# Kernel optimization log

Hardware: AMD Instinct MI355X
Metric: run time of the kernel (lower is better)

Reference implementation:

```python
import jax, jax.numpy as jnp
import numpy as np

N, E, D_IN, D_H, D_OUT, W = 100000, 1600000, 128, 128, 128, 3
HTC_W, TEMP = 0.01, 1.0  # curvature c = 1.0


def _project(x):
    n = jnp.maximum(jnp.linalg.norm(x, axis=-1, keepdims=True), 1e-12)
    return x * jnp.minimum((1.0 - 1e-5) / n, 1.0)


def _artanh(x):
    x = jnp.clip(x, -1.0 + 1e-6, 1.0 - 1e-6)
    return 0.5 * (jnp.log1p(x) - jnp.log1p(-x))


def _expmap0(v):
    n = jnp.maximum(jnp.linalg.norm(v, axis=-1, keepdims=True), 1e-12)
    return _project(jnp.tanh(n) * v / n)


def _logmap0(y):
    y = _project(y)
    n = jnp.maximum(jnp.linalg.norm(y, axis=-1, keepdims=True), 1e-12)
    return _artanh(n) * y / n


def setup_inputs() -> dict:
    key = jax.random.key(0)
    ks = jax.random.split(key, 24)
    x = jax.random.normal(ks[0], (N, D_IN), dtype=jnp.float32)
    edge_index = jax.random.randint(ks[1], (2, E), 0, N)
    t = jax.random.uniform(ks[2], (E,), dtype=jnp.float32)
    prev_hyp = _project(jax.random.normal(ks[3], (N, D_OUT), dtype=jnp.float32) * 0.05)
    lengths = jax.random.randint(ks[4], (N,), 0, W + 1)
    valid_mask = jnp.arange(W)[None, :] < lengths[:, None]  # front-filled deque
    hist_hyp = _project(jax.random.normal(ks[5], (N, W, D_OUT), dtype=jnp.float32) * 0.05)
    hist_hyp = hist_hyp * valid_mask[..., None].astype(jnp.float32)  # padded slots are zero

    def lin(k, dout, din):
        return jax.random.normal(k, (dout, din), dtype=jnp.float32) / np.sqrt(din)

    params = dict(
        w_time=jax.random.normal(ks[6], (D_IN,), dtype=jnp.float32),
        b_time=jnp.zeros((D_IN,), jnp.float32),
        W0_l=lin(ks[7], D_H, D_IN), b0_l=jnp.zeros((D_H,), jnp.float32), W0_r=lin(ks[8], D_H, D_IN),
        W1_l=lin(ks[9], D_OUT, D_H), b1_l=jnp.zeros((D_OUT,), jnp.float32), W1_r=lin(ks[10], D_OUT, D_H),
        W_ih=lin(ks[11], 3 * D_OUT, D_OUT), W_hh=lin(ks[12], 3 * D_OUT, D_OUT),
        b_ih=jnp.zeros((3 * D_OUT,), jnp.float32), b_hh=jnp.zeros((3 * D_OUT,), jnp.float32),
        Wq=lin(ks[13], D_OUT, D_OUT), Wk=lin(ks[14], D_OUT, D_OUT), Wv=lin(ks[15], D_OUT, D_OUT),
    )
    return dict(x=x, edge_index=edge_index, t=t, prev_hyp=prev_hyp,
                hist_hyp=hist_hyp, valid_mask=valid_mask, **params)


def reference(x, edge_index, t, prev_hyp, hist_hyp, valid_mask,
              w_time, b_time, W0_l, b0_l, W0_r, W1_l, b1_l, W1_r,
              W_ih, W_hh, b_ih, b_hh, Wq, Wk, Wv):
    n = x.shape[0]
    src, dst = edge_index[0], edge_index[1]
    ones_e = jnp.ones_like(t)
    # per-node mean event time over incident edges (src and dst both count)
    nt = jax.ops.segment_sum(t, src, n) + jax.ops.segment_sum(t, dst, n)
    cnt = jax.ops.segment_sum(ones_e, src, n) + jax.ops.segment_sum(ones_e, dst, n)
    node_time = nt / jnp.maximum(cnt, 1.0)
    x = x + jnp.cos(node_time[:, None] * w_time[None, :] + b_time[None, :])
    # SAGEConv (mean aggr over incoming edges): out = W_l @ mean_j x_j + b + W_r @ x_i
    deg = jnp.maximum(jax.ops.segment_sum(ones_e, dst, n), 1.0)[:, None]
    agg0 = jax.ops.segment_sum(x[src], dst, n) / deg
    h = jax.nn.relu(agg0 @ W0_l.T + b0_l + x @ W0_r.T)
    agg1 = jax.ops.segment_sum(h[src], dst, n) / deg
    h_now = agg1 @ W1_l.T + b1_l + h @ W1_r.T  # tangent-space current embedding

    prev_tan = _logmap0(prev_hyp)
    # ragged history attention (padded + masked)
    hist_tan = _logmap0(hist_hyp)                       # [N, W, D]
    q = h_now @ Wq.T                                    # [N, D]
    k = hist_tan @ Wk.T                                 # [N, W, D]
    v = hist_tan @ Wv.T
    score = jnp.einsum('nwd,nd->nw', k, q) / (np.sqrt(D_OUT) * max(TEMP, 1e-6))
    has_hist = valid_mask.any(axis=-1, keepdims=True)
    score = jnp.where(valid_mask, score, -jnp.inf)
    score = jnp.where(has_hist, score, 0.0)
    alpha = jax.nn.softmax(score, axis=-1)
    alpha = jnp.where(has_hist, alpha, 0.0)
    ctx = jnp.einsum('nw,nwd->nd', alpha, v)

    # GRUCell(input=h_now, hidden=prev_tan + ctx)
    hidden = prev_tan + ctx
    gi = h_now @ W_ih.T + b_ih
    gh = hidden @ W_hh.T + b_hh
    i_r, i_z, i_n = jnp.split(gi, 3, axis=-1)
    h_r, h_z, h_n = jnp.split(gh, 3, axis=-1)
    r = jax.nn.sigmoid(i_r + h_r)
    z = jax.nn.sigmoid(i_z + h_z)
    nn_ = jnp.tanh(i_n + r * h_n)
    h_tan = (1.0 - z) * nn_ + z * hidden
    h_hyp = _expmap0(h_tan)

    # hyperbolic temporal consistency aux loss (c = 1)
    x_sq = jnp.sum(h_hyp * h_hyp, axis=-1)
    y_sq = jnp.sum(prev_hyp * prev_hyp, axis=-1)
    diff_sq = jnp.sum((h_hyp - prev_hyp) ** 2, axis=-1)
    denom = jnp.maximum((1.0 - x_sq) * (1.0 - y_sq), 1e-8)
    zarg = jnp.maximum(1.0 + 2.0 * diff_sq / denom, 1.0 + 1e-6)
    dist = jnp.arccosh(zarg)
    valid_prev = (jnp.sum(jnp.abs(prev_hyp), axis=-1) > 0).astype(dist.dtype)
    aux = HTC_W * jnp.sum(dist * valid_prev) / jnp.maximum(jnp.sum(valid_prev), 1.0)
    aux = jnp.where(jnp.any(valid_prev > 0), aux, 0.0)
    return h_hyp, aux
```

## Files before the change

### kernel.cpp

```cpp
#include <hip/hip_runtime.h>
#include <math.h>


typedef _Float16 f16x8 __attribute__((ext_vector_type(8)));
typedef _Float16 f16x4 __attribute__((ext_vector_type(4)));
typedef _Float16 f16x2 __attribute__((ext_vector_type(2)));
typedef float f32x4 __attribute__((ext_vector_type(4)));

__device__ __forceinline__ float wsum(float v) {
#pragma unroll
  for (int off = 1; off < 64; off <<= 1) v += __shfl_xor(v, off, 64);
  return v;
}

__device__ __forceinline__ void fsplit(float x, _Float16& h, _Float16& l) {
  h = (_Float16)x;
  l = (_Float16)(x - (float)h);
}

__device__ __forceinline__ float logmap_scale(float nrm2) {
  float n0 = fmaxf(sqrtf(nrm2), 1e-12f);
  float sp = fminf((1.0f - 1e-5f) / n0, 1.0f);
  float np = fmaxf(n0 * sp, 1e-12f);
  float a  = fminf(np, 1.0f - 1e-6f);
  float at = 0.5f * (log1pf(a) - log1pf(-a));
  return sp * at / np;
}

__global__ void k_edge(const int* __restrict__ ei, const float* __restrict__ t,
                       unsigned long long* __restrict__ packed, int E) {
  int e = blockIdx.x * 256 + threadIdx.x;
  if (e >= E) return;
  int s = ei[e], d = ei[E + e];
  unsigned long long tf =
      (unsigned long long)__float2uint_rn(t[e] * 16777216.0f);
  unsigned long long encs = tf | (1ULL << 40);
  atomicAdd(&packed[s], encs);
  atomicAdd(&packed[d], encs | (1ULL << 52));
}

__global__ void k_scan1(const unsigned long long* __restrict__ packed,
                        int* __restrict__ rowptr, int* __restrict__ bsum, int N) {
  __shared__ int s[256];
  int t = threadIdx.x;
  int base = blockIdx.x * 1024 + t * 4;
  int v[4]; int loc = 0;
#pragma unroll
  for (int j = 0; j < 4; ++j) {
    int i = base + j;
    v[j] = (i < N) ? (int)(packed[i] >> 52) : 0;
    loc += v[j];
  }
  s[t] = loc; __syncthreads();
  for (int off = 1; off < 256; off <<= 1) {
    int x = (t >= off) ? s[t - off] : 0; __syncthreads();
    s[t] += x; __syncthreads();
  }
  int run = s[t] - loc;
#pragma unroll
  for (int j = 0; j < 4; ++j) { int i = base + j; if (i < N) rowptr[i] = run; run += v[j]; }
  if (t == 255) bsum[blockIdx.x] = s[255];
}

__global__ void k_scan2(const int* __restrict__ bsum, int* __restrict__ boff, int nb) {
  __shared__ int s[128];
  int t = threadIdx.x;
  int v = (t < nb) ? bsum[t] : 0;
  s[t] = v; __syncthreads();
  for (int off = 1; off < 128; off <<= 1) {
    int x = (t >= off) ? s[t - off] : 0; __syncthreads();
    s[t] += x; __syncthreads();
  }
  boff[t] = s[t] - v;
}

__global__ void k_scan3(int* __restrict__ rowptr, const int* __restrict__ boff, int N, int E) {
  int i = blockIdx.x * 256 + threadIdx.x;
  if (i < N) rowptr[i] += boff[i >> 10];
  if (i == 0) rowptr[N] = E;
}

__global__ void k_scatter(const int* __restrict__ ei, const int* __restrict__ rowptr,
                          int* __restrict__ cursor, int* __restrict__ eidx, int E) {
  int e = blockIdx.x * 256 + threadIdx.x;
  if (e >= E) return;
  int s = ei[e], d = ei[E + e];
  int p = rowptr[d] + atomicAdd(&cursor[d], 1);
  eidx[p] = s;
}

__global__ void k_time(const float* __restrict__ x,
                       const unsigned long long* __restrict__ packed,
                       const float* __restrict__ wt,
                       const float* __restrict__ bt, float* __restrict__ outF,
                       _Float16* __restrict__ outH, _Float16* __restrict__ outL, int N) {
  int id = blockIdx.x * 256 + threadIdx.x;
  if (id >= N * 32) return;
  int n = id >> 5, q = id & 31;
  unsigned long long p = packed[n];
  float tsum = (float)(p & 0xFFFFFFFFFFULL) * 5.9604644775390625e-8f;
  int c = (int)((p >> 40) & 0xFFF);
  float tm = tsum / fmaxf((float)c, 1.0f);
  float4 xv = ((const float4*)x)[id];
  float4 wv = ((const float4*)wt)[q];
  float4 bv = ((const float4*)bt)[q];
  float o[4];
  o[0] = xv.x + cosf(tm * wv.x + bv.x);
  o[1] = xv.y + cosf(tm * wv.y + bv.y);
  o[2] = xv.z + cosf(tm * wv.z + bv.z);
  o[3] = xv.w + cosf(tm * wv.w + bv.w);
  ((float4*)outF)[id] = make_float4(o[0], o[1], o[2], o[3]);
  f16x4 vh, vl;
#pragma unroll
  for (int j = 0; j < 4; ++j) { _Float16 h, l; fsplit(o[j], h, l); vh[j] = h; vl[j] = l; }
  *(f16x4*)&outH[(size_t)id * 4] = vh;
  *(f16x4*)&outL[(size_t)id * 4] = vl;
}

__global__ void k_agg(const float* __restrict__ X, const int* __restrict__ rowptr,
                      const int* __restrict__ eidx, _Float16* __restrict__ outH,
                      _Float16* __restrict__ outL, int N) {
  int wid = threadIdx.x >> 6, lane = threadIdx.x & 63;
  int n = blockIdx.x * 4 + wid;
  if (n >= N) return;
  int s0 = rowptr[n], s1 = rowptr[n + 1];
  float ax = 0.f, ay = 0.f;
  for (int e = s0; e < s1; ++e) {
    int s = eidx[e];
    float2 v = ((const float2*)X)[(size_t)s * 64 + lane];
    ax += v.x; ay += v.y;
  }
  float sc = 1.0f / fmaxf((float)(s1 - s0), 1.0f);
  _Float16 hx, lx, hy, ly;
  fsplit(ax * sc, hx, lx); fsplit(ay * sc, hy, ly);
  f16x2 vh = {hx, hy}, vl = {lx, ly};
  *(f16x2*)&outH[(size_t)n * 128 + lane * 2] = vh;
  *(f16x2*)&outL[(size_t)n * 128 + lane * 2] = vl;
}

__global__ void k_prep(const float* __restrict__ W0l, const float* __restrict__ W0r,
                       const float* __restrict__ W1l, const float* __restrict__ W1r,
                       const float* __restrict__ Wv,  const float* __restrict__ Wih,
                       const float* __restrict__ Whh, const float* __restrict__ bih,
                       const float* __restrict__ bhh,
                       _Float16* __restrict__ W0H, _Float16* __restrict__ W0L,
                       _Float16* __restrict__ W1H, _Float16* __restrict__ W1L,
                       _Float16* __restrict__ WvH, _Float16* __restrict__ WvL,
                       _Float16* __restrict__ WzH, _Float16* __restrict__ WzL,
                       float* __restrict__ bz) {
  int id = blockIdx.x * 256 + threadIdx.x;
  if (id < 32768) {
    int c = id >> 8, k = id & 255;
    float v0 = (k < 128) ? W0l[c * 128 + k] : W0r[c * 128 + (k - 128)];
    float v1 = (k < 128) ? W1l[c * 128 + k] : W1r[c * 128 + (k - 128)];
    fsplit(v0, W0H[id], W0L[id]);
    fsplit(v1, W1H[id], W1L[id]);
  }
  if (id < 16384) {
    fsplit(Wv[id], WvH[id], WvL[id]);
  }
  if (id < 131072) {
    int c = id >> 8, k = id & 255;
    float v;
    if (c < 256)      v = (k < 128) ? Wih[c * 128 + k] : Whh[c * 128 + (k - 128)];
    else if (c < 384) v = (k < 128) ? Wih[c * 128 + k] : 0.f;
    else              v = (k < 128) ? 0.f : Whh[(c - 128) * 128 + (k - 128)];
    fsplit(v, WzH[id], WzL[id]);
  }
  if (id < 512) {
    float v;
    if (id < 256)      v = bih[id] + bhh[id];
    else if (id < 384) v = bih[id];
    else               v = bhh[id - 128];
    bz[id] = v;
  }
}

__global__ void k_ct(const float* __restrict__ Wk, const float* __restrict__ Wq,
                     _Float16* __restrict__ CtH, _Float16* __restrict__ CtL) {
  int id = blockIdx.x * 256 + threadIdx.x;
  if (id >= 16384) return;
  int c = id >> 7, k = id & 127;
  float s = 0.f;
  for (int j = 0; j < 128; ++j) s += Wk[j * 128 + c] * Wq[j * 128 + k];
  fsplit(s, CtH[id], CtL[id]);
}

__global__ __launch_bounds__(256)
void k_mm(const _Float16* __restrict__ A1H, const _Float16* __restrict__ A1L,
          const _Float16* __restrict__ A2H, const _Float16* __restrict__ A2L,
          const _Float16* __restrict__ WH,  const _Float16* __restrict__ WL,
          const float* __restrict__ bias,   const float* __restrict__ addb,
          float* __restrict__ outF, _Float16* __restrict__ outH,
          _Float16* __restrict__ outL,
          int Nrows, int Ktot, int Ctot, int relu) {
  __shared__ _Float16 sA[2][128][64];
  __shared__ _Float16 sW[2][128][64];
  const int tid = threadIdx.x;
  const int lane = tid & 63;
  const int wv = tid >> 6;
  const int wr = wv >> 1, wc = wv & 1;
  const int laneR = lane & 15, laneG = lane >> 4;
  const int n0 = blockIdx.x * 128;
  const int c0 = blockIdx.y * 128;

  f32x4 acc[4][4];
#pragma unroll
  for (int mi = 0; mi < 4; ++mi)
#pragma unroll
    for (int ni = 0; ni < 4; ++ni)
#pragma unroll
      for (int j = 0; j < 4; ++j) acc[mi][ni][j] = 0.f;

  const int nslab = Ktot >> 6;
  for (int s = 0; s < nslab; ++s) {
    int kglob = s << 6;
    const _Float16* aH = (kglob < 128) ? A1H : A2H;
    const _Float16* aL = (kglob < 128) ? A1L : A2L;
    int kc = kglob & 127;
    __syncthreads();
#pragma unroll
    for (int it = 0; it < 4; ++it) {
      int idx = tid + (it << 8);
      int r = idx >> 3, chunk = idx & 7;
      int cs = (chunk ^ (r & 7)) << 3;
      int kq = chunk << 3;
      int n = n0 + r;
      f16x8 vh, vl;
      if (n < Nrows) {
        vh = *(const f16x8*)&aH[(size_t)n * 128 + kc + kq];
        vl = *(const f16x8*)&aL[(size_t)n * 128 + kc + kq];
      } else {
#pragma unroll
        for (int j = 0; j < 8; ++j) { vh[j] = (_Float16)0; vl[j] = (_Float16)0; }
      }
      *(f16x8*)&sA[0][r][cs] = vh;
      *(f16x8*)&sA[1][r][cs] = vl;
      int c = c0 + r;
      f16x8 wh = *(const f16x8*)&WH[(size_t)c * Ktot + kglob + kq];
      f16x8 wl = *(const f16x8*)&WL[(size_t)c * Ktot + kglob + kq];
      *(f16x8*)&sW[0][r][cs] = wh;
      *(f16x8*)&sW[1][r][cs] = wl;
    }
    __syncthreads();
#pragma unroll
    for (int kk = 0; kk < 2; ++kk) {
      f16x8 ah[4], al[4], bh[4], bl[4];
      int kch = (kk << 2) + laneG;
#pragma unroll
      for (int m = 0; m < 4; ++m) {
        int row = wr * 64 + m * 16 + laneR;
        int ko = (kch ^ (row & 7)) << 3;
        ah[m] = *(const f16x8*)&sA[0][row][ko];
        al[m] = *(const f16x8*)&sA[1][row][ko];
      }
#pragma unroll
      for (int n = 0; n < 4; ++n) {
        int row = wc * 64 + n * 16 + laneR;
        int ko = (kch ^ (row & 7)) << 3;
        bh[n] = *(const f16x8*)&sW[0][row][ko];
        bl[n] = *(const f16x8*)&sW[1][row][ko];
      }
#pragma unroll
      for (int m = 0; m < 4; ++m)
#pragma unroll
        for (int n = 0; n < 4; ++n) {
          acc[m][n] = __builtin_amdgcn_mfma_f32_16x16x32_f16(ah[m], bh[n], acc[m][n], 0, 0, 0);
          acc[m][n] = __builtin_amdgcn_mfma_f32_16x16x32_f16(al[m], bh[n], acc[m][n], 0, 0, 0);
          acc[m][n] = __builtin_amdgcn_mfma_f32_16x16x32_f16(ah[m], bl[n], acc[m][n], 0, 0, 0);
        }
    }
  }
#pragma unroll
  for (int m = 0; m < 4; ++m) {
#pragma unroll
    for (int n = 0; n < 4; ++n) {
      int rbase = n0 + wr * 64 + m * 16 + laneG * 4;
      int c = c0 + wc * 64 + n * 16 + laneR;
      float bval = bias ? bias[c] : 0.f;
#pragma unroll
      for (int j = 0; j < 4; ++j) {
        int r = rbase + j;
        if (r >= Nrows) continue;
        float v = acc[m][n][j] + bval;
        if (addb) v += addb[(size_t)r * Ctot + c];
        if (relu) v = fmaxf(v, 0.f);
        if (outF) outF[(size_t)r * Ctot + c] = v;
        if (outH) {
          _Float16 h, l; fsplit(v, h, l);
          outH[(size_t)r * Ctot + c] = h;
          outL[(size_t)r * Ctot + c] = l;
        }
      }
    }
  }
}

__global__ __launch_bounds__(256, 2)
void k_gru(const _Float16* __restrict__ P0H, const _Float16* __restrict__ P0L,
           const _Float16* __restrict__ P2H, const _Float16* __restrict__ P2L,
           const _Float16* __restrict__ WzH, const _Float16* __restrict__ WzL,
           const float* __restrict__ bz, const float* __restrict__ prev,
           float* __restrict__ out, float* __restrict__ pd,
           float* __restrict__ pv, int N) {
  __shared__ _Float16 sA[2][64][64];
  __shared__ float rn1[64][2];
  __shared__ float rn3[64][2][3];
  __shared__ float distrow[64], validrow[64];
  const int tid = threadIdx.x;
  const int lane = tid & 63;
  const int wv = tid >> 6;
  const int wr = wv >> 1, wc = wv & 1;
  const int laneR = lane & 15, laneG = lane >> 4;
  const int n0 = blockIdx.x * 64;

  f32x4 acc[4][2][4];
#pragma unroll
  for (int q = 0; q < 4; ++q)
#pragma unroll
    for (int m = 0; m < 2; ++m)
#pragma unroll
      for (int n = 0; n < 4; ++n)
#pragma unroll
        for (int j = 0; j < 4; ++j) acc[q][m][n][j] = 0.f;

#define COMPUTE_Q(Q)                                                        \
  {                                                                         \
    _Pragma("unroll")                                                       \
    for (int kk = 0; kk < 2; ++kk) {                                        \
      int kch = (kk << 2) + laneG;                                          \
      f16x8 ah[2], al[2], bh[4], bl[4];                                     \
      _Pragma("unroll")                                                     \
      for (int n = 0; n < 4; ++n) {                                         \
        size_t wrow = (size_t)((Q) * 128 + wc * 64 + n * 16 + laneR);       \
        size_t o = wrow * 256 + kglob + (kch << 3);                         \
        bh[n] = *(const f16x8*)&WzH[o];                                     \
        bl[n] = *(const f16x8*)&WzL[o];                                     \
      }                                                                     \
      _Pragma("unroll")                                                     \
      for (int m = 0; m < 2; ++m) {                                         \
        int row = wr * 32 + m * 16 + laneR;                                 \
        int ko = (kch ^ (row & 7)) << 3;                                    \
        ah[m] = *(const f16x8*)&sA[0][row][ko];                             \
        al[m] = *(const f16x8*)&sA[1][row][ko];                             \
      }                                                                     \
      _Pragma("unroll")                                                     \
      for (int m = 0; m < 2; ++m)                                           \
        _Pragma("unroll")                                                   \
        for (int n = 0; n < 4; ++n) {                                       \
          acc[Q][m][n] = __builtin_amdgcn_mfma_f32_16x16x32_f16(ah[m], bh[n], acc[Q][m][n], 0, 0, 0); \
          acc[Q][m][n] = __builtin_amdgcn_mfma_f32_16x16x32_f16(al[m], bh[n], acc[Q][m][n], 0, 0, 0); \
          acc[Q][m][n] = __builtin_amdgcn_mfma_f32_16x16x32_f16(ah[m], bl[n], acc[Q][m][n], 0, 0, 0); \
        }                                                                   \
    }                                                                       \
  }

#pragma unroll
  for (int s = 0; s < 4; ++s) {
    int kglob = s << 6;
    const _Float16* aH = (s < 2) ? P0H : P2H;
    const _Float16* aL = (s < 2) ? P0L : P2L;
    int kc = kglob & 127;
    __syncthreads();
#pragma unroll
    for (int it = 0; it < 2; ++it) {
      int idx = tid + (it << 8);
      int r = idx >> 3, chunk = idx & 7;
      int cs = (chunk ^ (r & 7)) << 3;
      int kq = chunk << 3;
      int n = n0 + r;
      f16x8 vh, vl;
      if (n < N) {
        vh = *(const f16x8*)&aH[(size_t)n * 128 + kc + kq];
        vl = *(const f16x8*)&aL[(size_t)n * 128 + kc + kq];
      } else {
#pragma unroll
        for (int j = 0; j < 8; ++j) { vh[j] = (_Float16)0; vl[j] = (_Float16)0; }
      }
      *(f16x8*)&sA[0][r][cs] = vh;
      *(f16x8*)&sA[1][r][cs] = vl;
    }
    __syncthreads();
    COMPUTE_Q(0);
    COMPUTE_Q(1);
    if (s < 2) {
      COMPUTE_Q(2);
    } else {
      COMPUTE_Q(3);
    }
  }
#undef COMPUTE_Q

  float bz0[4], bz1[4], bz2[4], bz3[4];
#pragma unroll
  for (int n = 0; n < 4; ++n) {
    int d = wc * 64 + n * 16 + laneR;
    bz0[n] = bz[d]; bz1[n] = bz[128 + d]; bz2[n] = bz[256 + d]; bz3[n] = bz[384 + d];
  }
  float tv[2][4][4];
#pragma unroll
  for (int m = 0; m < 2; ++m)
#pragma unroll
    for (int n = 0; n < 4; ++n)
#pragma unroll
      for (int j = 0; j < 4; ++j) {
        int row = n0 + wr * 32 + m * 16 + laneG * 4 + j;
        int d = wc * 64 + n * 16 + laneR;
        float hid = 0.f;
        if (row < N) {
          size_t o = (size_t)row * 128 + d;
          hid = (float)P2H[o] + (float)P2L[o];
        }
        float gr = acc[0][m][n][j] + bz0[n];
        float gz = acc[1][m][n][j] + bz1[n];
        float gi = acc[2][m][n][j] + bz2[n];
        float gh = acc[3][m][n][j] + bz3[n];
        float rr = 1.f / (1.f + expf(-gr));
        float zz = 1.f / (1.f + expf(-gz));
        float nn = tanhf(gi + rr * gh);
        tv[m][n][j] = (1.f - zz) * nn + zz * hid;
      }
#pragma unroll
  for (int m = 0; m < 2; ++m)
#pragma unroll
    for (int j = 0; j < 4; ++j) {
      float p = 0.f;
#pragma unroll
      for (int n = 0; n < 4; ++n) p += tv[m][n][j] * tv[m][n][j];
#pragma unroll
      for (int off = 1; off < 16; off <<= 1) p += __shfl_xor(p, off, 64);
      if (laneR == 0) rn1[wr * 32 + m * 16 + laneG * 4 + j][wc] = p;
    }
  __syncthreads();
  float hv[2][4][4];
#pragma unroll
  for (int m = 0; m < 2; ++m)
#pragma unroll
    for (int j = 0; j < 4; ++j) {
      int rl = wr * 32 + m * 16 + laneG * 4 + j;
      int row = n0 + rl;
      float nv2 = rn1[rl][0] + rn1[rl][1];
      float nv = fmaxf(sqrtf(nv2), 1e-12f);
      float tn = tanhf(nv);
      float s1 = tn / nv;
      float nw = fmaxf(tn, 1e-12f);
      float sp = fminf((1.f - 1e-5f) / nw, 1.f);
      float scl = s1 * sp;
#pragma unroll
      for (int n = 0; n < 4; ++n) {
        float h = tv[m][n][j] * scl;
        hv[m][n][j] = h;
        int d = wc * 64 + n * 16 + laneR;
        if (row < N) out[(size_t)row * 128 + d] = h;
      }
    }
#pragma unroll
  for (int m = 0; m < 2; ++m)
#pragma unroll
    for (int j = 0; j < 4; ++j) {
      int rl = wr * 32 + m * 16 + laneG * 4 + j;
      int row = n0 + rl;
      float ys = 0.f, ds = 0.f, pa = 0.f;
#pragma unroll
      for (int n = 0; n < 4; ++n) {
        int d = wc * 64 + n * 16 + laneR;
        float p = (row < N) ? prev[(size_t)row * 128 + d] : 0.f;
        float h = hv[m][n][j];
        ys += p * p; ds += (h - p) * (h - p); pa += fabsf(p);
      }
#pragma unroll
      for (int off = 1; off < 16; off <<= 1) {
        ys += __shfl_xor(ys, off, 64);
        ds += __shfl_xor(ds, off, 64);
        pa += __shfl_xor(pa, off, 64);
      }
      if (laneR == 0) { rn3[rl][wc][0] = ys; rn3[rl][wc][1] = ds; rn3[rl][wc][2] = pa; }
    }
  __syncthreads();
  if (wc == 0 && laneR == 0) {
#pragma unroll
    for (int m = 0; m < 2; ++m)
#pragma unroll
      for (int j = 0; j < 4; ++j) {
        int rl = wr * 32 + m * 16 + laneG * 4 + j;
        int row = n0 + rl;
        float nv2 = rn1[rl][0] + rn1[rl][1];
        float nv = fmaxf(sqrtf(nv2), 1e-12f);
        float tn = tanhf(nv);
        float s1 = tn / nv;
        float nw = fmaxf(tn, 1e-12f);
        float sp = fminf((1.f - 1e-5f) / nw, 1.f);
        float scl = s1 * sp;
        float x_sq = scl * scl * nv2;
        float y_sq = rn3[rl][0][0] + rn3[rl][1][0];
        float d_sq = rn3[rl][0][1] + rn3[rl][1][1];
        float pab  = rn3[rl][0][2] + rn3[rl][1][2];
        float denom = fmaxf((1.f - x_sq) * (1.f - y_sq), 1e-8f);
        float zarg = fmaxf(1.f + 2.f * d_sq / denom, 1.f + 1e-6f);
        float dist = acoshf(zarg);
        float valid = (pab > 0.f && row < N) ? 1.f : 0.f;
        distrow[rl] = dist * valid;
        validrow[rl] = valid;
      }
  }
  __syncthreads();
  if (tid < 64) {
    float dv = distrow[tid], vvv = validrow[tid];
    dv = wsum(dv); vvv = wsum(vvv);
    if (tid == 0) { pd[blockIdx.x] = dv; pv[blockIdx.x] = vvv; }
  }
}

__global__ void k_logmap(const float* __restrict__ Y, float* __restrict__ out, int N) {
  int wid = threadIdx.x >> 6, lane = threadIdx.x & 63;
  int n = blockIdx.x * 4 + wid;
  if (n >= N) return;
  float2 y = ((const float2*)Y)[(size_t)n * 64 + lane];
  float nrm2 = wsum(y.x * y.x + y.y * y.y);
  float s = logmap_scale(nrm2);
  ((float2*)out)[(size_t)n * 64 + lane] = make_float2(y.x * s, y.y * s);
}

__global__ void k_attn(const float* __restrict__ U, const float* __restrict__ hist,
                       _Float16* __restrict__ outH, _Float16* __restrict__ outL, int N) {
  int wid = threadIdx.x >> 6, lane = threadIdx.x & 63;
  int n = blockIdx.x * 4 + wid;
  if (n >= N) return;
  float2 u = ((const float2*)U)[(size_t)n * 64 + lane];
  float htx[3], hty[3], sc[3];
  bool val[3];
#pragma unroll
  for (int w = 0; w < 3; ++w) {
    float2 h = ((const float2*)hist)[((size_t)n * 3 + w) * 64 + lane];
    float nrm2 = wsum(h.x * h.x + h.y * h.y);
    val[w] = nrm2 > 0.f;
    float s = logmap_scale(nrm2);
    htx[w] = h.x * s; hty[w] = h.y * s;
    float d = wsum(htx[w] * u.x + hty[w] * u.y);
    sc[w] = d * 0.0883883476483184f;
  }
  float cx = 0.f, cy = 0.f;
  if (val[0] || val[1] || val[2]) {
    float m = -INFINITY;
#pragma unroll
    for (int w = 0; w < 3; ++w) if (val[w]) m = fmaxf(m, sc[w]);
    float a[3]; float ssum = 0.f;
#pragma unroll
    for (int w = 0; w < 3; ++w) { a[w] = val[w] ? expf(sc[w] - m) : 0.f; ssum += a[w]; }
    float inv = 1.f / ssum;
#pragma unroll
    for (int w = 0; w < 3; ++w) { cx += htx[w] * (a[w] * inv); cy += hty[w] * (a[w] * inv); }
  }
  _Float16 hx, lx, hy, ly;
  fsplit(cx, hx, lx); fsplit(cy, hy, ly);
  f16x2 vh = {hx, hy}, vl = {lx, ly};
  *(f16x2*)&outH[(size_t)n * 128 + lane * 2] = vh;
  *(f16x2*)&outL[(size_t)n * 128 + lane * 2] = vl;
}

__global__ void k_reduce(const float* __restrict__ pd, const float* __restrict__ pv,
                         float* __restrict__ aux_out, int nparts) {
  __shared__ float sd[256], sv[256];
  float a = 0.f, b = 0.f;
  for (int i = threadIdx.x; i < nparts; i += 256) { a += pd[i]; b += pv[i]; }
  sd[threadIdx.x] = a; sv[threadIdx.x] = b; __syncthreads();
  for (int off = 128; off > 0; off >>= 1) {
    if (threadIdx.x < off) { sd[threadIdx.x] += sd[threadIdx.x + off]; sv[threadIdx.x] += sv[threadIdx.x + off]; }
    __syncthreads();
  }
  if (threadIdx.x == 0) {
    float aux = (sv[0] > 0.f) ? 0.01f * sd[0] / fmaxf(sv[0], 1.f) : 0.f;
    aux_out[0] = aux;
  }
}

extern "C" void kernel_launch(void* const* d_in, const int* in_sizes, int n_in,
                              void* d_out, int out_size, void* d_ws, size_t ws_size,
                              hipStream_t stream) {
  const float* x      = (const float*)d_in[0];
  const int*   ei     = (const int*)  d_in[1];
  const float* t      = (const float*)d_in[2];
  const float* prev   = (const float*)d_in[3];
  const float* hist   = (const float*)d_in[4];
  const float* w_time = (const float*)d_in[6];
  const float* b_time = (const float*)d_in[7];
  const float* W0l    = (const float*)d_in[8];
  const float* b0l    = (const float*)d_in[9];
  const float* W0r    = (const float*)d_in[10];
  const float* W1l    = (const float*)d_in[11];
  const float* b1l    = (const float*)d_in[12];
  const float* W1r    = (const float*)d_in[13];
  const float* Wih    = (const float*)d_in[14];
  const float* Whh    = (const float*)d_in[15];
  const float* bih    = (const float*)d_in[16];
  const float* bhh    = (const float*)d_in[17];
  const float* Wq     = (const float*)d_in[18];
  const float* Wk     = (const float*)d_in[19];
  const float* Wv     = (const float*)d_in[20];

  const int N = in_sizes[0] / 128;
  const int E = in_sizes[1] / 2;
  const int NB4 = (N + 3) / 4;
  const int NB1 = (N + 1023) / 1024;
  const int NBG = (N + 63) / 64;

  char* wbase = (char*)d_ws;
  size_t off = 0;
  auto alloc = [&](size_t bytes) -> void* {
    off = (off + 255) & ~(size_t)255;
    void* p = wbase + off; off += bytes; return p;
  };
  unsigned long long* packed = (unsigned long long*)alloc((size_t)N * 8);
  int*   cursor = (int*)  alloc((size_t)N * 4);
  size_t zero_bytes = off;
  int*   rowptr = (int*)  alloc((size_t)(N + 1) * 4);
  int*   bsum   = (int*)  alloc(512);
  int*   boff   = (int*)  alloc(512);
  int*   eidx   = (int*)  alloc((size_t)E * 4);
  _Float16* W0H = (_Float16*)alloc(32768 * 2);
  _Float16* W0L = (_Float16*)alloc(32768 * 2);
  _Float16* W1H = (_Float16*)alloc(32768 * 2);
  _Float16* W1L = (_Float16*)alloc(32768 * 2);
  _Float16* CtH = (_Float16*)alloc(16384 * 2);
  _Float16* CtL = (_Float16*)alloc(16384 * 2);
  _Float16* WvH = (_Float16*)alloc(16384 * 2);
  _Float16* WvL = (_Float16*)alloc(16384 * 2);
  _Float16* WzH = (_Float16*)alloc(131072 * 2);
  _Float16* WzL = (_Float16*)alloc(131072 * 2);
  float* bz     = (float*)alloc(512 * 4);
  float* F0 = (float*)alloc((size_t)N * 128 * 4);
  float* F1 = (float*)alloc((size_t)N * 128 * 4);
  _Float16* P0H = (_Float16*)alloc((size_t)N * 128 * 2);
  _Float16* P0L = (_Float16*)alloc((size_t)N * 128 * 2);
  _Float16* P1H = (_Float16*)alloc((size_t)N * 128 * 2);
  _Float16* P1L = (_Float16*)alloc((size_t)N * 128 * 2);
  _Float16* P2H = (_Float16*)alloc((size_t)N * 128 * 2);
  _Float16* P2L = (_Float16*)alloc((size_t)N * 128 * 2);
  float* pd = (float*)alloc((size_t)NBG * 4);
  float* pv = (float*)alloc((size_t)NBG * 4);
  (void)ws_size; (void)n_in; (void)out_size;

  float* out_h   = (float*)d_out;
  float* out_aux = out_h + (size_t)N * 128;

  hipMemsetAsync(d_ws, 0, zero_bytes, stream);

  k_prep<<<512, 256, 0, stream>>>(W0l, W0r, W1l, W1r, Wv, Wih, Whh, bih, bhh,
                                  W0H, W0L, W1H, W1L, WvH, WvL, WzH, WzL, bz);
  k_ct<<<64, 256, 0, stream>>>(Wk, Wq, CtH, CtL);

  int ebl = (E + 255) / 256;
  k_edge<<<ebl, 256, 0, stream>>>(ei, t, packed, E);
  k_scan1<<<NB1, 256, 0, stream>>>(packed, rowptr, bsum, N);
  k_scan2<<<1, 128, 0, stream>>>(bsum, boff, NB1);
  k_scan3<<<(N + 255) / 256, 256, 0, stream>>>(rowptr, boff, N, E);
  k_scatter<<<ebl, 256, 0, stream>>>(ei, rowptr, cursor, eidx, E);

  k_time<<<(N * 32 + 255) / 256, 256, 0, stream>>>(x, packed, w_time, b_time,
                                                   F0, P0H, P0L, N);
  k_agg<<<NB4, 256, 0, stream>>>(F0, rowptr, eidx, P1H, P1L, N);
  dim3 gb((N + 127) / 128, 1);
  k_mm<<<gb, 256, 0, stream>>>(P1H, P1L, P0H, P0L, W0H, W0L, b0l, nullptr,
                               F1, P2H, P2L, N, 256, 128, 1);
  k_agg<<<NB4, 256, 0, stream>>>(F1, rowptr, eidx, P1H, P1L, N);
  k_mm<<<gb, 256, 0, stream>>>(P1H, P1L, P2H, P2L, W1H, W1L, b1l, nullptr,
                               nullptr, P0H, P0L, N, 256, 128, 0);
  k_mm<<<gb, 256, 0, stream>>>(P0H, P0L, nullptr, nullptr, CtH, CtL, nullptr, nullptr,
                               F0, nullptr, nullptr, N, 128, 128, 0);
  k_attn<<<NB4, 256, 0, stream>>>(F0, hist, P1H, P1L, N);
  k_logmap<<<NB4, 256, 0, stream>>>(prev, F1, N);
  k_mm<<<gb, 256, 0, stream>>>(P1H, P1L, nullptr, nullptr, WvH, WvL, nullptr, F1,
                               nullptr, P2H, P2L, N, 128, 128, 0);
  k_gru<<<NBG, 256, 0, stream>>>(P0H, P0L, P2H, P2L, WzH, WzL, bz, prev,
                                 out_h, pd, pv, N);
  k_reduce<<<1, 256, 0, stream>>>(pd, pv, out_aux, NBG);
}
```

Measured before the change: 1.315 ms.

## Gather aggregation from split fp16 buffers and stage GRU weights in LDS

```diff
diff --git a/kernel.cpp b/kernel.cpp
--- a/kernel.cpp
+++ b/kernel.cpp
@@ -92,7 +92,7 @@
 __global__ void k_time(const float* __restrict__ x,
                        const unsigned long long* __restrict__ packed,
                        const float* __restrict__ wt,
-                       const float* __restrict__ bt, float* __restrict__ outF,
+                       const float* __restrict__ bt,
                        _Float16* __restrict__ outH, _Float16* __restrict__ outL, int N) {
   int id = blockIdx.x * 256 + threadIdx.x;
   if (id >= N * 32) return;
@@ -109,7 +109,6 @@
   o[1] = xv.y + cosf(tm * wv.y + bv.y);
   o[2] = xv.z + cosf(tm * wv.z + bv.z);
   o[3] = xv.w + cosf(tm * wv.w + bv.w);
-  ((float4*)outF)[id] = make_float4(o[0], o[1], o[2], o[3]);
   f16x4 vh, vl;
 #pragma unroll
   for (int j = 0; j < 4; ++j) { _Float16 h, l; fsplit(o[j], h, l); vh[j] = h; vl[j] = l; }
@@ -117,7 +116,8 @@
   *(f16x4*)&outL[(size_t)id * 4] = vl;
 }
 
-__global__ void k_agg(const float* __restrict__ X, const int* __restrict__ rowptr,
+__global__ void k_agg(const _Float16* __restrict__ XH, const _Float16* __restrict__ XL,
+                      const int* __restrict__ rowptr,
                       const int* __restrict__ eidx, _Float16* __restrict__ outH,
                       _Float16* __restrict__ outL, int N) {
   int wid = threadIdx.x >> 6, lane = threadIdx.x & 63;
@@ -127,8 +127,10 @@
   float ax = 0.f, ay = 0.f;
   for (int e = s0; e < s1; ++e) {
     int s = eidx[e];
-    float2 v = ((const float2*)X)[(size_t)s * 64 + lane];
-    ax += v.x; ay += v.y;
+    f16x2 vh = *(const f16x2*)&XH[(size_t)s * 128 + lane * 2];
+    f16x2 vl = *(const f16x2*)&XL[(size_t)s * 128 + lane * 2];
+    ax += (float)vh[0] + (float)vl[0];
+    ay += (float)vh[1] + (float)vl[1];
   }
   float sc = 1.0f / fmaxf((float)(s1 - s0), 1.0f);
   _Float16 hx, lx, hy, ly;
@@ -304,6 +306,7 @@
            float* __restrict__ out, float* __restrict__ pd,
            float* __restrict__ pv, int N) {
   __shared__ _Float16 sA[2][64][64];
+  __shared__ _Float16 sW[2][128][64];
   __shared__ float rn1[64][2];
   __shared__ float rn3[64][2][3];
   __shared__ float distrow[64], validrow[64];
@@ -324,6 +327,20 @@
 #pragma unroll
         for (int j = 0; j < 4; ++j) acc[q][m][n][j] = 0.f;
 
+#define STAGE_W(Q)                                                          \
+  {                                                                         \
+    _Pragma("unroll")                                                       \
+    for (int it = 0; it < 4; ++it) {                                        \
+      int idx = tid + (it << 8);                                            \
+      int r = idx >> 3, chunk = idx & 7;                                    \
+      int cs = (chunk ^ (r & 7)) << 3;                                      \
+      int kq = chunk << 3;                                                  \
+      size_t wrow = (size_t)((Q)*128 + r);                                  \
+      *(f16x8*)&sW[0][r][cs] = *(const f16x8*)&WzH[wrow * 256 + kglob + kq];\
+      *(f16x8*)&sW[1][r][cs] = *(const f16x8*)&WzL[wrow * 256 + kglob + kq];\
+    }                                                                       \
+  }
+
 #define COMPUTE_Q(Q)                                                        \
   {                                                                         \
     _Pragma("unroll")                                                       \
@@ -331,18 +348,18 @@
       int kch = (kk << 2) + laneG;                                          \
       f16x8 ah[2], al[2], bh[4], bl[4];                                     \
       _Pragma("unroll")                                                     \
-      for (int n = 0; n < 4; ++n) {                                         \
-        size_t wrow = (size_t)((Q) * 128 + wc * 64 + n * 16 + laneR);       \
-        size_t o = wrow * 256 + kglob + (kch << 3);                         \
-        bh[n] = *(const f16x8*)&WzH[o];                                     \
-        bl[n] = *(const f16x8*)&WzL[o];                                     \
-      }                                                                     \
-      _Pragma("unroll")                                                     \
       for (int m = 0; m < 2; ++m) {                                         \
         int row = wr * 32 + m * 16 + laneR;                                 \
         int ko = (kch ^ (row & 7)) << 3;                                    \
         ah[m] = *(const f16x8*)&sA[0][row][ko];                             \
         al[m] = *(const f16x8*)&sA[1][row][ko];                             \
+      }                                                                     \
+      _Pragma("unroll")                                                     \
+      for (int n = 0; n < 4; ++n) {                                         \
+        int row = wc * 64 + n * 16 + laneR;                                 \
+        int ko = (kch ^ (row & 7)) << 3;                                    \
+        bh[n] = *(const f16x8*)&sW[0][row][ko];                             \
+        bl[n] = *(const f16x8*)&sW[1][row][ko];                             \
       }                                                                     \
       _Pragma("unroll")                                                     \
       for (int m = 0; m < 2; ++m)                                           \
@@ -380,15 +397,25 @@
       *(f16x8*)&sA[0][r][cs] = vh;
       *(f16x8*)&sA[1][r][cs] = vl;
     }
+    STAGE_W(0);
     __syncthreads();
     COMPUTE_Q(0);
+    __syncthreads();
+    STAGE_W(1);
+    __syncthreads();
     COMPUTE_Q(1);
+    __syncthreads();
     if (s < 2) {
+      STAGE_W(2);
+      __syncthreads();
       COMPUTE_Q(2);
     } else {
+      STAGE_W(3);
+      __syncthreads();
       COMPUTE_Q(3);
     }
   }
+#undef STAGE_W
 #undef COMPUTE_Q
 
   float bz0[4], bz1[4], bz2[4], bz3[4];
@@ -657,12 +684,12 @@
   k_scatter<<<ebl, 256, 0, stream>>>(ei, rowptr, cursor, eidx, E);
 
   k_time<<<(N * 32 + 255) / 256, 256, 0, stream>>>(x, packed, w_time, b_time,
-                                                   F0, P0H, P0L, N);
-  k_agg<<<NB4, 256, 0, stream>>>(F0, rowptr, eidx, P1H, P1L, N);
+                                                   P0H, P0L, N);
+  k_agg<<<NB4, 256, 0, stream>>>(P0H, P0L, rowptr, eidx, P1H, P1L, N);
   dim3 gb((N + 127) / 128, 1);
   k_mm<<<gb, 256, 0, stream>>>(P1H, P1L, P0H, P0L, W0H, W0L, b0l, nullptr,
-                               F1, P2H, P2L, N, 256, 128, 1);
-  k_agg<<<NB4, 256, 0, stream>>>(F1, rowptr, eidx, P1H, P1L, N);
+                               nullptr, P2H, P2L, N, 256, 128, 1);
+  k_agg<<<NB4, 256, 0, stream>>>(P2H, P2L, rowptr, eidx, P1H, P1L, N);
   k_mm<<<gb, 256, 0, stream>>>(P1H, P1L, P2H, P2L, W1H, W1L, b1l, nullptr,
                                nullptr, P0H, P0L, N, 256, 128, 0);
   k_mm<<<gb, 256, 0, stream>>>(P0H, P0L, nullptr, nullptr, CtH, CtL, nullptr, nullptr,
```

After: 1.224 ms. 1.07x faster.
